# Optimization experiments

Measured on AMD Instinct MI355X. Metric: run time of the kernel, lower is better.

## Reference

```python
import jax, jax.numpy as jnp
import numpy as np

N_NODES = 50000
N_EDGES = 800000
NODE_FEATURES = 128
HIDDEN = 64
N_CLASSES = 6


def gcn_conv(x, src, dst, W, b, n_nodes):
    """PyG GCNConv: out = D^{-1/2}(A+I)D^{-1/2} X W + b (self-loops included)."""
    deg = jax.ops.segment_sum(jnp.ones_like(dst, dtype=x.dtype), dst, num_segments=n_nodes)
    dinv = jnp.where(deg > 0, jax.lax.rsqrt(deg), 0.0)  # [N]
    h = x @ W  # [N, out] - transform before gather (fewer bytes moved)
    norm = dinv[src] * dinv[dst]  # [E+N]
    msg = h[src] * norm[:, None]  # [E+N, out]
    out = jax.ops.segment_sum(msg, dst, num_segments=n_nodes)  # [N, out]
    return out + b


def setup_inputs() -> dict:
    key = jax.random.key(0)
    ks = jax.random.split(key, 8)
    x = jax.random.normal(ks[0], (N_NODES, NODE_FEATURES), dtype=jnp.float32)
    edge_index = jax.random.randint(ks[1], (2, N_EDGES), 0, N_NODES, dtype=jnp.int64)
    W1 = jax.random.normal(ks[2], (NODE_FEATURES, HIDDEN), dtype=jnp.float32) * (1.0 / np.sqrt(NODE_FEATURES))
    b1 = jnp.zeros((HIDDEN,), dtype=jnp.float32)
    W2 = jax.random.normal(ks[3], (HIDDEN, HIDDEN), dtype=jnp.float32) * (1.0 / np.sqrt(HIDDEN))
    b2 = jnp.zeros((HIDDEN,), dtype=jnp.float32)
    Wc = jax.random.normal(ks[4], (HIDDEN * N_NODES, N_CLASSES), dtype=jnp.float32) * (1.0 / np.sqrt(HIDDEN * N_NODES))
    bc = jnp.zeros((N_CLASSES,), dtype=jnp.float32)
    return {"x": x, "edge_index": edge_index, "W1": W1, "b1": b1, "W2": W2, "b2": b2, "Wc": Wc, "bc": bc}


def reference(x, edge_index, W1, b1, W2, b2, Wc, bc):
    n_nodes = x.shape[0]
    loops = jnp.arange(n_nodes, dtype=edge_index.dtype)
    src = jnp.concatenate([edge_index[0], loops])
    dst = jnp.concatenate([edge_index[1], loops])
    h = jax.nn.relu(gcn_conv(x, src, dst, W1, b1, n_nodes))
    h = jax.nn.relu(gcn_conv(h, src, dst, W2, b2, n_nodes))
    logits = h.reshape(1, -1) @ Wc + bc  # [1, n_classes]
    return jax.nn.softmax(logits, axis=1)
```

## Files before the change

kernel.cpp:

```cpp
#include <hip/hip_runtime.h>
#include <math.h>


#define NCH 256
#define RBITS 10
#define NR_MAX 64

__device__ __forceinline__ ushort f32_to_bf16(float f) {
  unsigned u = __float_as_uint(f);
  return (ushort)((u + 0x7fffu + ((u >> 16) & 1u)) >> 16);
}
__device__ __forceinline__ float bf16_to_f32(ushort h) {
  return __uint_as_float(((unsigned)h) << 16);
}


__global__ __launch_bounds__(256) void hist_ranges(
    const int* __restrict__ dst, int* __restrict__ ghist, int NR, int E) {
  __shared__ int h[NR_MAX];
  int tid = threadIdx.x, c = blockIdx.x;
  if (tid < NR) h[tid] = 0;
  __syncthreads();
  int E4 = E >> 2;
  int CH4 = (E4 + NCH - 1) / NCH;
  int i0 = c * CH4, i1 = min(i0 + CH4, E4);
  const int4* d4 = (const int4*)dst;
  for (int i = i0 + tid; i < i1; i += 256) {
    int4 d = d4[i];
    atomicAdd(&h[d.x >> RBITS], 1);
    atomicAdd(&h[d.y >> RBITS], 1);
    atomicAdd(&h[d.z >> RBITS], 1);
    atomicAdd(&h[d.w >> RBITS], 1);
  }
  if (c == NCH - 1) {
    for (int e = (E4 << 2) + tid; e < E; e += 256) atomicAdd(&h[dst[e] >> RBITS], 1);
  }
  __syncthreads();
  if (tid < NR) ghist[tid * NCH + c] = h[tid];
}


__global__ __launch_bounds__(1024) void scan_ghist(int* __restrict__ g, int M) {
  __shared__ int wtot[16];
  int tid = threadIdx.x, lane = tid & 63, wv = tid >> 6;
  int SEG = (M + 1023) >> 10;
  int base = tid * SEG;
  int s = 0;
  for (int k = 0; k < SEG; ++k) { int i = base + k; if (i < M) s += g[i]; }
  int x = s;
#pragma unroll
  for (int d = 1; d < 64; d <<= 1) { int y = __shfl_up(x, d, 64); if (lane >= d) x += y; }
  if (lane == 63) wtot[wv] = x;
  __syncthreads();
  if (wv == 0 && lane < 16) {
    int t = wtot[lane], xx = t;
#pragma unroll
    for (int d = 1; d < 16; d <<= 1) { int y = __shfl_up(xx, d, 64); if (lane >= d) xx += y; }
    wtot[lane] = xx - t;
  }
  __syncthreads();
  int run = x - s + wtot[wv];
  for (int k = 0; k < SEG; ++k) {
    int i = base + k;
    if (i < M) { int tmp = g[i]; g[i] = run; run += tmp; }
  }
}


__global__ __launch_bounds__(256) void scatter_ranges(
    const int* __restrict__ src, const int* __restrict__ dst,
    const int* __restrict__ ghist, int2* __restrict__ ebuf, int NR, int E) {
  __shared__ int cur[NR_MAX];
  int tid = threadIdx.x, c = blockIdx.x;
  if (tid < NR) cur[tid] = ghist[tid * NCH + c];
  __syncthreads();
  int E4 = E >> 2;
  int CH4 = (E4 + NCH - 1) / NCH;
  int i0 = c * CH4, i1 = min(i0 + CH4, E4);
  const int4* d4 = (const int4*)dst;
  const int4* s4 = (const int4*)src;
  for (int i = i0 + tid; i < i1; i += 256) {
    int4 d = d4[i];
    int4 s = s4[i];
    ebuf[atomicAdd(&cur[d.x >> RBITS], 1)] = make_int2(s.x, d.x);
    ebuf[atomicAdd(&cur[d.y >> RBITS], 1)] = make_int2(s.y, d.y);
    ebuf[atomicAdd(&cur[d.z >> RBITS], 1)] = make_int2(s.z, d.z);
    ebuf[atomicAdd(&cur[d.w >> RBITS], 1)] = make_int2(s.w, d.w);
  }
  if (c == NCH - 1) {
    for (int e = (E4 << 2) + tid; e < E; e += 256)
      ebuf[atomicAdd(&cur[dst[e] >> RBITS], 1)] = make_int2(src[e], dst[e]);
  }
}


__global__ __launch_bounds__(1024) void csr_range(
    const int2* __restrict__ ebuf, const int* __restrict__ ghist,
    int* __restrict__ offs, int* __restrict__ srt, float* __restrict__ dinv,
    int N, int E, int NR) {
  __shared__ int hist[1024];
  __shared__ int wtot[16];
  int r = blockIdx.x;
  int lo = r << RBITS;
  int len = min(1024, N - lo);
  int tid = threadIdx.x, lane = tid & 63, wv = tid >> 6;
  int S  = ghist[r * NCH];
  int S1 = (r + 1 < NR) ? ghist[(r + 1) * NCH] : E;
  if (tid < len) hist[tid] = 0;
  __syncthreads();
  for (int i = S + tid; i < S1; i += 1024) atomicAdd(&hist[ebuf[i].y - lo], 1);
  __syncthreads();
  int v = (tid < len) ? hist[tid] : 0;
  if (tid < len) dinv[lo + tid] = rsqrtf((float)(v + 1));
  int x = v;
#pragma unroll
  for (int d = 1; d < 64; d <<= 1) { int y = __shfl_up(x, d, 64); if (lane >= d) x += y; }
  if (lane == 63) wtot[wv] = x;
  __syncthreads();
  if (wv == 0 && lane < 16) {
    int t = wtot[lane], xx = t;
#pragma unroll
    for (int d = 1; d < 16; d <<= 1) { int y = __shfl_up(xx, d, 64); if (lane >= d) xx += y; }
    wtot[lane] = xx - t;
  }
  __syncthreads();
  int excl = x - v + wtot[wv];
  if (tid < len) {
    offs[lo + tid] = S + excl;
    hist[tid] = S + excl;
  }
  if (r == 0 && tid == 0) offs[N] = E;
  __syncthreads();
  for (int i = S + tid; i < S1; i += 1024) {
    int2 e = ebuf[i];
    srt[atomicAdd(&hist[e.y - lo], 1)] = e.x;
  }
}


template <int K, int ROWS>
__global__ __launch_bounds__(256) void gemm_scale(
    const float* __restrict__ X, const float* __restrict__ W,
    const float* __restrict__ dinv, ushort* __restrict__ Gb, int N) {
  __shared__ float smw[K * 64];
  __shared__ float xs[ROWS * K];
  int tid = threadIdx.x, lane = tid & 63, wv = tid >> 6;
  for (int idx = tid; idx < K * 16; idx += 256)
    ((float4*)smw)[idx] = ((const float4*)W)[idx];
  int row0 = blockIdx.x * ROWS;
  int base = row0 * K;
  int cnt4 = (min(ROWS * K, N * K - base)) >> 2;
  const float4* X4 = (const float4*)(X + base);
  for (int idx = tid; idx < cnt4; idx += 256) ((float4*)xs)[idx] = X4[idx];
  __syncthreads();

  constexpr int RW = ROWS / 4;
  float acc[RW];
#pragma unroll
  for (int r = 0; r < RW; ++r) acc[r] = 0.f;
  const float* xr = &xs[(wv * RW) * K];
#pragma unroll 4
  for (int k = 0; k < K; ++k) {
    float wval = smw[k * 64 + lane];
#pragma unroll
    for (int r = 0; r < RW; ++r) acc[r] = fmaf(xr[r * K + k], wval, acc[r]);
  }
#pragma unroll
  for (int r = 0; r < RW; ++r) {
    int row = row0 + wv * RW + r;
    if (row < N) Gb[(size_t)row * 64 + lane] = f32_to_bf16(acc[r] * dinv[row]);
  }
}


__global__ __launch_bounds__(256) void aggregate(
    const ushort* __restrict__ Gb, const int* __restrict__ offs,
    const int* __restrict__ srt, const float* __restrict__ dinv,
    const float* __restrict__ bias, float* __restrict__ H, int N) {
  int lane = threadIdx.x & 63, wv = threadIdx.x >> 6;
  int sub = lane >> 4, fl = lane & 15;
  int node = blockIdx.x * 4 + wv;
  if (node >= N) return;
  const ushort4* G2 = (const ushort4*)Gb;

  int e0 = offs[node], e1 = offs[node + 1];
  int deg = e1 - e0;

  float4 accA = make_float4(0.f, 0.f, 0.f, 0.f);
  float4 accB = make_float4(0.f, 0.f, 0.f, 0.f);
  if (sub == 0) {
    ushort4 q = G2[(size_t)node * 16 + fl];
    accA.x = bf16_to_f32(q.x); accA.y = bf16_to_f32(q.y);
    accA.z = bf16_to_f32(q.z); accA.w = bf16_to_f32(q.w);
  }

  int pre = (deg > 0) ? srt[e0 + min(lane, deg - 1)] : 0;

  int dcap = min(deg, 64);
  int base = 0;
  for (; base + 7 < dcap; base += 8) {
    int sA = __shfl(pre, base + sub, 64);
    int sB = __shfl(pre, base + 4 + sub, 64);
    ushort4 qA = G2[(size_t)sA * 16 + fl];
    ushort4 qB = G2[(size_t)sB * 16 + fl];
    accA.x += bf16_to_f32(qA.x); accA.y += bf16_to_f32(qA.y);
    accA.z += bf16_to_f32(qA.z); accA.w += bf16_to_f32(qA.w);
    accB.x += bf16_to_f32(qB.x); accB.y += bf16_to_f32(qB.y);
    accB.z += bf16_to_f32(qB.z); accB.w += bf16_to_f32(qB.w);
  }
  for (; base + 3 < dcap; base += 4) {
    int s = __shfl(pre, base + sub, 64);
    ushort4 q = G2[(size_t)s * 16 + fl];
    accA.x += bf16_to_f32(q.x); accA.y += bf16_to_f32(q.y);
    accA.z += bf16_to_f32(q.z); accA.w += bf16_to_f32(q.w);
  }
  int e = e0 + base;
  for (; e + 3 < e1; e += 4) {
    int s = srt[e + sub];
    ushort4 q = G2[(size_t)s * 16 + fl];
    accA.x += bf16_to_f32(q.x); accA.y += bf16_to_f32(q.y);
    accA.z += bf16_to_f32(q.z); accA.w += bf16_to_f32(q.w);
  }
  int rem = e1 - e;
  if (sub < rem) {
    int s = srt[e + sub];
    ushort4 q = G2[(size_t)s * 16 + fl];
    accA.x += bf16_to_f32(q.x); accA.y += bf16_to_f32(q.y);
    accA.z += bf16_to_f32(q.z); accA.w += bf16_to_f32(q.w);
  }

  float4 acc;
  acc.x = accA.x + accB.x; acc.y = accA.y + accB.y;
  acc.z = accA.z + accB.z; acc.w = accA.w + accB.w;
#pragma unroll
  for (int m = 16; m < 64; m <<= 1) {
    acc.x += __shfl_xor(acc.x, m, 64);
    acc.y += __shfl_xor(acc.y, m, 64);
    acc.z += __shfl_xor(acc.z, m, 64);
    acc.w += __shfl_xor(acc.w, m, 64);
  }
  if (sub == 0) {
    float dn = dinv[node];
    float4 bb = ((const float4*)bias)[fl];
    float4 r;
    r.x = fmaxf(fmaf(acc.x, dn, bb.x), 0.f);
    r.y = fmaxf(fmaf(acc.y, dn, bb.y), 0.f);
    r.z = fmaxf(fmaf(acc.z, dn, bb.z), 0.f);
    r.w = fmaxf(fmaf(acc.w, dn, bb.w), 0.f);
    ((float4*)H)[(size_t)node * 16 + fl] = r;
  }
}


__global__ __launch_bounds__(256) void classifier(
    const float* __restrict__ H, const float* __restrict__ Wc,
    float* __restrict__ part, int M12) {
  float a[6] = {0.f, 0.f, 0.f, 0.f, 0.f, 0.f};
  int stride = gridDim.x * blockDim.x;
  for (int g = blockIdx.x * blockDim.x + threadIdx.x; g < M12; g += stride) {
    const float4* w4 = (const float4*)Wc + (size_t)g * 3;
    float4 v0 = w4[0];
    float4 v1 = w4[1];
    float4 v2 = w4[2];
    float2 h = ((const float2*)H)[g];
    a[0] = fmaf(h.x, v0.x, a[0]); a[1] = fmaf(h.x, v0.y, a[1]);
    a[2] = fmaf(h.x, v0.z, a[2]); a[3] = fmaf(h.x, v0.w, a[3]);
    a[4] = fmaf(h.x, v1.x, a[4]); a[5] = fmaf(h.x, v1.y, a[5]);
    a[0] = fmaf(h.y, v1.z, a[0]); a[1] = fmaf(h.y, v1.w, a[1]);
    a[2] = fmaf(h.y, v2.x, a[2]); a[3] = fmaf(h.y, v2.y, a[3]);
    a[4] = fmaf(h.y, v2.z, a[4]); a[5] = fmaf(h.y, v2.w, a[5]);
  }
#pragma unroll
  for (int c = 0; c < 6; ++c) {
    for (int d = 32; d > 0; d >>= 1) a[c] += __shfl_down(a[c], d, 64);
  }
  __shared__ float sh[4][6];
  int lane = threadIdx.x & 63, wv = threadIdx.x >> 6;
  if (lane == 0) {
#pragma unroll
    for (int c = 0; c < 6; ++c) sh[wv][c] = a[c];
  }
  __syncthreads();
  if (threadIdx.x == 0) {
#pragma unroll
    for (int c = 0; c < 6; ++c)
      part[(size_t)blockIdx.x * 6 + c] = sh[0][c] + sh[1][c] + sh[2][c] + sh[3][c];
  }
}

__global__ __launch_bounds__(256) void reduce_softmax(
    const float* __restrict__ part, int nb,
    const float* __restrict__ bc, float* __restrict__ out) {
  int tid = threadIdx.x, lane = tid & 63, wv = tid >> 6;
  float a[6] = {0.f, 0.f, 0.f, 0.f, 0.f, 0.f};
  for (int b = tid; b < nb; b += 256) {
    const float* p = part + (size_t)b * 6;
#pragma unroll
    for (int c = 0; c < 6; ++c) a[c] += p[c];
  }
#pragma unroll
  for (int c = 0; c < 6; ++c) {
    for (int d = 32; d > 0; d >>= 1) a[c] += __shfl_down(a[c], d, 64);
  }
  __shared__ float sh[4][6];
  if (lane == 0) {
#pragma unroll
    for (int c = 0; c < 6; ++c) sh[wv][c] = a[c];
  }
  __syncthreads();
  if (tid == 0) {
    float l[6], m = -1e30f;
#pragma unroll
    for (int c = 0; c < 6; ++c) {
      l[c] = sh[0][c] + sh[1][c] + sh[2][c] + sh[3][c] + bc[c];
      m = fmaxf(m, l[c]);
    }
    float s = 0.f;
#pragma unroll
    for (int c = 0; c < 6; ++c) { l[c] = __expf(l[c] - m); s += l[c]; }
    float inv = 1.f / s;
#pragma unroll
    for (int c = 0; c < 6; ++c) out[c] = l[c] * inv;
  }
}


static inline size_t align4up(size_t x) { return (x + 3) & ~(size_t)3; }

extern "C" void kernel_launch(void* const* d_in, const int* in_sizes, int n_in,
                              void* d_out, int out_size, void* d_ws, size_t ws_size,
                              hipStream_t stream) {
  const float* x  = (const float*)d_in[0];
  const int*   ei = (const int*)d_in[1];
  const float* W1 = (const float*)d_in[2];
  const float* b1 = (const float*)d_in[3];
  const float* W2 = (const float*)d_in[4];
  const float* b2 = (const float*)d_in[5];
  const float* Wc = (const float*)d_in[6];
  const float* bc = (const float*)d_in[7];
  float* out = (float*)d_out;

  const int N = in_sizes[0] / 128;
  const int E = in_sizes[1] / 2;
  const int* esrc = ei;
  const int* edst = ei + E;
  const int NR = (N + 1023) >> RBITS;
  const int CGRID = 2048;

  size_t o = 0;
  int* offs   = (int*)d_ws + o;           o = align4up(o + N + 1);
  int* srt    = (int*)d_ws + o;           o = align4up(o + E);
  float* dinv = (float*)d_ws + o;         o = align4up(o + N);
  int* ghist  = (int*)d_ws + o;           o = align4up(o + (size_t)NR * NCH);
  ushort* Gb  = (ushort*)((int*)d_ws + o); o = align4up(o + (size_t)N * 32);
  float* bufB = (float*)d_ws + o;         o = align4up(o + (size_t)N * 64);
  float* part = (float*)d_ws + o;         o = align4up(o + (size_t)CGRID * 6);
  int2* ebuf  = (int2*)bufB;

  hist_ranges<<<NCH, 256, 0, stream>>>(edst, ghist, NR, E);
  scan_ghist<<<1, 1024, 0, stream>>>(ghist, NR * NCH);
  scatter_ranges<<<NCH, 256, 0, stream>>>(esrc, edst, ghist, ebuf, NR, E);
  csr_range<<<NR, 1024, 0, stream>>>(ebuf, ghist, offs, srt, dinv, N, E, NR);

  gemm_scale<128, 32><<<(N + 31) / 32, 256, 0, stream>>>(x, W1, dinv, Gb, N);
  aggregate<<<(N + 3) / 4, 256, 0, stream>>>(Gb, offs, srt, dinv, b1, bufB, N);
  gemm_scale<64, 32><<<(N + 31) / 32, 256, 0, stream>>>(bufB, W2, dinv, Gb, N);
  aggregate<<<(N + 3) / 4, 256, 0, stream>>>(Gb, offs, srt, dinv, b2, bufB, N);

  classifier<<<CGRID, 256, 0, stream>>>(bufB, Wc, part, N * 32);
  reduce_softmax<<<1, 256, 0, stream>>>(part, CGRID, bc, out);
}
```

Before: 165.9 us.

## Split aggregation into two passes by source-node half for cache locality

Each node's CSR neighbor list is partitioned by whether the source index falls in the lower or upper half of nodes, and a split offset is recorded per node. Aggregation then runs as two kernels, the first over low-half sources writing partial fp32 sums and the second over high-half sources accumulating and applying dinv, bias and ReLU. The intent is that each pass gathers from only half of the bf16 feature table (~3.2MB), improving cache hit rates for the random gathers. The cost is extra launches, an fp32 partial-sum write and read per node, and more atomics in CSR construction.

```diff
diff --git a/kernel.cpp b/kernel.cpp
--- a/kernel.cpp
+++ b/kernel.cpp
@@ -96,9 +96,10 @@
 
 __global__ __launch_bounds__(1024) void csr_range(
     const int2* __restrict__ ebuf, const int* __restrict__ ghist,
-    int* __restrict__ offs, int* __restrict__ srt, float* __restrict__ dinv,
-    int N, int E, int NR) {
-  __shared__ int hist[1024];
+    int* __restrict__ offs, int* __restrict__ splits, int* __restrict__ srt,
+    float* __restrict__ dinv, int N, int E, int NR, int NHALF) {
+  __shared__ int hT[1024];
+  __shared__ int hL[1024];
   __shared__ int wtot[16];
   int r = blockIdx.x;
   int lo = r << RBITS;
@@ -106,11 +107,15 @@
   int tid = threadIdx.x, lane = tid & 63, wv = tid >> 6;
   int S  = ghist[r * NCH];
   int S1 = (r + 1 < NR) ? ghist[(r + 1) * NCH] : E;
-  if (tid < len) hist[tid] = 0;
-  __syncthreads();
-  for (int i = S + tid; i < S1; i += 1024) atomicAdd(&hist[ebuf[i].y - lo], 1);
-  __syncthreads();
-  int v = (tid < len) ? hist[tid] : 0;
+  if (tid < len) { hT[tid] = 0; hL[tid] = 0; }
+  __syncthreads();
+  for (int i = S + tid; i < S1; i += 1024) {
+    int2 e = ebuf[i];
+    atomicAdd(&hT[e.y - lo], 1);
+    if (e.x < NHALF) atomicAdd(&hL[e.y - lo], 1);
+  }
+  __syncthreads();
+  int v = (tid < len) ? hT[tid] : 0;
   if (tid < len) dinv[lo + tid] = rsqrtf((float)(v + 1));
   int x = v;
 #pragma unroll
@@ -126,14 +131,20 @@
   __syncthreads();
   int excl = x - v + wtot[wv];
   if (tid < len) {
-    offs[lo + tid] = S + excl;
-    hist[tid] = S + excl;
+    int base = S + excl;
+    int sp = base + hL[tid];
+    offs[lo + tid] = base;
+    splits[lo + tid] = sp;
+    hT[tid] = base;
+    hL[tid] = sp;
   }
   if (r == 0 && tid == 0) offs[N] = E;
   __syncthreads();
   for (int i = S + tid; i < S1; i += 1024) {
     int2 e = ebuf[i];
-    srt[atomicAdd(&hist[e.y - lo], 1)] = e.x;
+    int idx = e.y - lo;
+    int p = (e.x < NHALF) ? atomicAdd(&hT[idx], 1) : atomicAdd(&hL[idx], 1);
+    srt[p] = e.x;
   }
 }
 
@@ -173,25 +184,33 @@
 }
 
 
+template <int PASS>
 __global__ __launch_bounds__(256) void aggregate(
     const ushort* __restrict__ Gb, const int* __restrict__ offs,
-    const int* __restrict__ srt, const float* __restrict__ dinv,
-    const float* __restrict__ bias, float* __restrict__ H, int N) {
+    const int* __restrict__ splits, const int* __restrict__ srt,
+    const float* __restrict__ dinv, const float* __restrict__ bias,
+    float* __restrict__ H, int N) {
   int lane = threadIdx.x & 63, wv = threadIdx.x >> 6;
   int sub = lane >> 4, fl = lane & 15;
   int node = blockIdx.x * 4 + wv;
   if (node >= N) return;
   const ushort4* G2 = (const ushort4*)Gb;
 
-  int e0 = offs[node], e1 = offs[node + 1];
+  int e0, e1;
+  if (PASS == 0) { e0 = offs[node]; e1 = splits[node]; }
+  else           { e0 = splits[node]; e1 = offs[node + 1]; }
   int deg = e1 - e0;
 
   float4 accA = make_float4(0.f, 0.f, 0.f, 0.f);
   float4 accB = make_float4(0.f, 0.f, 0.f, 0.f);
   if (sub == 0) {
-    ushort4 q = G2[(size_t)node * 16 + fl];
-    accA.x = bf16_to_f32(q.x); accA.y = bf16_to_f32(q.y);
-    accA.z = bf16_to_f32(q.z); accA.w = bf16_to_f32(q.w);
+    if (PASS == 0) {
+      ushort4 q = G2[(size_t)node * 16 + fl];
+      accA.x = bf16_to_f32(q.x); accA.y = bf16_to_f32(q.y);
+      accA.z = bf16_to_f32(q.z); accA.w = bf16_to_f32(q.w);
+    } else {
+      accA = ((const float4*)H)[(size_t)node * 16 + fl];
+    }
   }
 
   int pre = (deg > 0) ? srt[e0 + min(lane, deg - 1)] : 0;
@@ -240,14 +259,18 @@
     acc.w += __shfl_xor(acc.w, m, 64);
   }
   if (sub == 0) {
-    float dn = dinv[node];
-    float4 bb = ((const float4*)bias)[fl];
-    float4 r;
-    r.x = fmaxf(fmaf(acc.x, dn, bb.x), 0.f);
-    r.y = fmaxf(fmaf(acc.y, dn, bb.y), 0.f);
-    r.z = fmaxf(fmaf(acc.z, dn, bb.z), 0.f);
-    r.w = fmaxf(fmaf(acc.w, dn, bb.w), 0.f);
-    ((float4*)H)[(size_t)node * 16 + fl] = r;
+    if (PASS == 0) {
+      ((float4*)H)[(size_t)node * 16 + fl] = acc;
+    } else {
+      float dn = dinv[node];
+      float4 bb = ((const float4*)bias)[fl];
+      float4 r;
+      r.x = fmaxf(fmaf(acc.x, dn, bb.x), 0.f);
+      r.y = fmaxf(fmaf(acc.y, dn, bb.y), 0.f);
+      r.z = fmaxf(fmaf(acc.z, dn, bb.z), 0.f);
+      r.w = fmaxf(fmaf(acc.w, dn, bb.w), 0.f);
+      ((float4*)H)[(size_t)node * 16 + fl] = r;
+    }
   }
 }
 
@@ -346,9 +369,11 @@
   const int* edst = ei + E;
   const int NR = (N + 1023) >> RBITS;
   const int CGRID = 2048;
+  const int NHALF = (N / 2 + 3) & ~3;
 
   size_t o = 0;
   int* offs   = (int*)d_ws + o;           o = align4up(o + N + 1);
+  int* splits = (int*)d_ws + o;           o = align4up(o + N);
   int* srt    = (int*)d_ws + o;           o = align4up(o + E);
   float* dinv = (float*)d_ws + o;         o = align4up(o + N);
   int* ghist  = (int*)d_ws + o;           o = align4up(o + (size_t)NR * NCH);
@@ -360,12 +385,15 @@
   hist_ranges<<<NCH, 256, 0, stream>>>(edst, ghist, NR, E);
   scan_ghist<<<1, 1024, 0, stream>>>(ghist, NR * NCH);
   scatter_ranges<<<NCH, 256, 0, stream>>>(esrc, edst, ghist, ebuf, NR, E);
-  csr_range<<<NR, 1024, 0, stream>>>(ebuf, ghist, offs, srt, dinv, N, E, NR);
-
+  csr_range<<<NR, 1024, 0, stream>>>(ebuf, ghist, offs, splits, srt, dinv, N, E, NR, NHALF);
+
+  const int AGRID = (N + 3) / 4;
   gemm_scale<128, 32><<<(N + 31) / 32, 256, 0, stream>>>(x, W1, dinv, Gb, N);
-  aggregate<<<(N + 3) / 4, 256, 0, stream>>>(Gb, offs, srt, dinv, b1, bufB, N);
+  aggregate<0><<<AGRID, 256, 0, stream>>>(Gb, offs, splits, srt, dinv, b1, bufB, N);
+  aggregate<1><<<AGRID, 256, 0, stream>>>(Gb, offs, splits, srt, dinv, b1, bufB, N);
   gemm_scale<64, 32><<<(N + 31) / 32, 256, 0, stream>>>(bufB, W2, dinv, Gb, N);
-  aggregate<<<(N + 3) / 4, 256, 0, stream>>>(Gb, offs, srt, dinv, b2, bufB, N);
+  aggregate<0><<<AGRID, 256, 0, stream>>>(Gb, offs, splits, srt, dinv, b2, bufB, N);
+  aggregate<1><<<AGRID, 256, 0, stream>>>(Gb, offs, splits, srt, dinv, b2, bufB, N);
 
   classifier<<<CGRID, 256, 0, stream>>>(bufB, Wc, part, N * 32);
   reduce_softmax<<<1, 256, 0, stream>>>(part, CGRID, bc, out);
```

Result: slower. 188.7 us (+13.8%).

## Fuse classifier dot product into second aggregation kernel epilogue

Applied to the files above, without the earlier changes.

The second GCN aggregation now applies the bias and ReLU and immediately multiplies each node's 64 features by the matching Wc rows. It reduces the per-block partial logits inside the block and writes them to a partial buffer. This removes the write and re-read of the second-layer hidden matrix and one kernel launch. In exchange the final reduction must sum about 12.5k partials instead of 2048, so it is widened to 1024 threads. Each block also now pays extra shuffle reductions and a __syncthreads.

```diff
diff --git a/kernel.cpp b/kernel.cpp
--- a/kernel.cpp
+++ b/kernel.cpp
@@ -173,22 +173,26 @@
 }
 
 
+template <int CLS>
 __global__ __launch_bounds__(256) void aggregate(
     const ushort* __restrict__ Gb, const int* __restrict__ offs,
     const int* __restrict__ srt, const float* __restrict__ dinv,
-    const float* __restrict__ bias, float* __restrict__ H, int N) {
+    const float* __restrict__ bias, const float* __restrict__ Wc,
+    float* __restrict__ H, float* __restrict__ part, int N) {
   int lane = threadIdx.x & 63, wv = threadIdx.x >> 6;
   int sub = lane >> 4, fl = lane & 15;
   int node = blockIdx.x * 4 + wv;
-  if (node >= N) return;
   const ushort4* G2 = (const ushort4*)Gb;
 
-  int e0 = offs[node], e1 = offs[node + 1];
+  if (CLS == 0 && node >= N) return;
+
+  int e0 = 0, e1 = 0;
+  if (node < N) { e0 = offs[node]; e1 = offs[node + 1]; }
   int deg = e1 - e0;
 
   float4 accA = make_float4(0.f, 0.f, 0.f, 0.f);
   float4 accB = make_float4(0.f, 0.f, 0.f, 0.f);
-  if (sub == 0) {
+  if (sub == 0 && node < N) {
     ushort4 q = G2[(size_t)node * 16 + fl];
     accA.x = bf16_to_f32(q.x); accA.y = bf16_to_f32(q.y);
     accA.z = bf16_to_f32(q.z); accA.w = bf16_to_f32(q.w);
@@ -239,61 +243,61 @@
     acc.z += __shfl_xor(acc.z, m, 64);
     acc.w += __shfl_xor(acc.w, m, 64);
   }
-  if (sub == 0) {
-    float dn = dinv[node];
-    float4 bb = ((const float4*)bias)[fl];
-    float4 r;
-    r.x = fmaxf(fmaf(acc.x, dn, bb.x), 0.f);
-    r.y = fmaxf(fmaf(acc.y, dn, bb.y), 0.f);
-    r.z = fmaxf(fmaf(acc.z, dn, bb.z), 0.f);
-    r.w = fmaxf(fmaf(acc.w, dn, bb.w), 0.f);
-    ((float4*)H)[(size_t)node * 16 + fl] = r;
-  }
-}
-
-
-__global__ __launch_bounds__(256) void classifier(
-    const float* __restrict__ H, const float* __restrict__ Wc,
-    float* __restrict__ part, int M12) {
-  float a[6] = {0.f, 0.f, 0.f, 0.f, 0.f, 0.f};
-  int stride = gridDim.x * blockDim.x;
-  for (int g = blockIdx.x * blockDim.x + threadIdx.x; g < M12; g += stride) {
-    const float4* w4 = (const float4*)Wc + (size_t)g * 3;
-    float4 v0 = w4[0];
-    float4 v1 = w4[1];
-    float4 v2 = w4[2];
-    float2 h = ((const float2*)H)[g];
-    a[0] = fmaf(h.x, v0.x, a[0]); a[1] = fmaf(h.x, v0.y, a[1]);
-    a[2] = fmaf(h.x, v0.z, a[2]); a[3] = fmaf(h.x, v0.w, a[3]);
-    a[4] = fmaf(h.x, v1.x, a[4]); a[5] = fmaf(h.x, v1.y, a[5]);
-    a[0] = fmaf(h.y, v1.z, a[0]); a[1] = fmaf(h.y, v1.w, a[1]);
-    a[2] = fmaf(h.y, v2.x, a[2]); a[3] = fmaf(h.y, v2.y, a[3]);
-    a[4] = fmaf(h.y, v2.z, a[4]); a[5] = fmaf(h.y, v2.w, a[5]);
-  }
-#pragma unroll
-  for (int c = 0; c < 6; ++c) {
-    for (int d = 32; d > 0; d >>= 1) a[c] += __shfl_down(a[c], d, 64);
-  }
-  __shared__ float sh[4][6];
-  int lane = threadIdx.x & 63, wv = threadIdx.x >> 6;
-  if (lane == 0) {
-#pragma unroll
-    for (int c = 0; c < 6; ++c) sh[wv][c] = a[c];
-  }
-  __syncthreads();
-  if (threadIdx.x == 0) {
-#pragma unroll
-    for (int c = 0; c < 6; ++c)
-      part[(size_t)blockIdx.x * 6 + c] = sh[0][c] + sh[1][c] + sh[2][c] + sh[3][c];
-  }
-}
-
-__global__ __launch_bounds__(256) void reduce_softmax(
+
+  if (CLS == 0) {
+    if (sub == 0 && node < N) {
+      float dn = dinv[node];
+      float4 bb = ((const float4*)bias)[fl];
+      float4 r;
+      r.x = fmaxf(fmaf(acc.x, dn, bb.x), 0.f);
+      r.y = fmaxf(fmaf(acc.y, dn, bb.y), 0.f);
+      r.z = fmaxf(fmaf(acc.z, dn, bb.z), 0.f);
+      r.w = fmaxf(fmaf(acc.w, dn, bb.w), 0.f);
+      ((float4*)H)[(size_t)node * 16 + fl] = r;
+    }
+  } else {
+    float a[6] = {0.f, 0.f, 0.f, 0.f, 0.f, 0.f};
+    if (sub == 0 && node < N) {
+      float dn = dinv[node];
+      float4 bb = ((const float4*)bias)[fl];
+      float4 r;
+      r.x = fmaxf(fmaf(acc.x, dn, bb.x), 0.f);
+      r.y = fmaxf(fmaf(acc.y, dn, bb.y), 0.f);
+      r.z = fmaxf(fmaf(acc.z, dn, bb.z), 0.f);
+      r.w = fmaxf(fmaf(acc.w, dn, bb.w), 0.f);
+      const float4* w4 = (const float4*)(Wc + (size_t)node * 384 + fl * 24);
+      float4 w0 = w4[0], w1 = w4[1], w2 = w4[2], w3 = w4[3], w4_ = w4[4], w5 = w4[5];
+      a[0] = fmaf(r.x, w0.x, fmaf(r.y, w1.z, fmaf(r.z, w3.x, r.w * w4_.z)));
+      a[1] = fmaf(r.x, w0.y, fmaf(r.y, w1.w, fmaf(r.z, w3.y, r.w * w4_.w)));
+      a[2] = fmaf(r.x, w0.z, fmaf(r.y, w2.x, fmaf(r.z, w3.z, r.w * w5.x)));
+      a[3] = fmaf(r.x, w0.w, fmaf(r.y, w2.y, fmaf(r.z, w3.w, r.w * w5.y)));
+      a[4] = fmaf(r.x, w1.x, fmaf(r.y, w2.z, fmaf(r.z, w4_.x, r.w * w5.z)));
+      a[5] = fmaf(r.x, w1.y, fmaf(r.y, w2.w, fmaf(r.z, w4_.y, r.w * w5.w)));
+    }
+#pragma unroll
+    for (int c = 0; c < 6; ++c) {
+      for (int d = 32; d > 0; d >>= 1) a[c] += __shfl_down(a[c], d, 64);
+    }
+    __shared__ float sh[4][6];
+    if (lane == 0) {
+#pragma unroll
+      for (int c = 0; c < 6; ++c) sh[wv][c] = a[c];
+    }
+    __syncthreads();
+    if (threadIdx.x == 0) {
+#pragma unroll
+      for (int c = 0; c < 6; ++c)
+        part[(size_t)blockIdx.x * 6 + c] = sh[0][c] + sh[1][c] + sh[2][c] + sh[3][c];
+    }
+  }
+}
+
+__global__ __launch_bounds__(1024) void reduce_softmax(
     const float* __restrict__ part, int nb,
     const float* __restrict__ bc, float* __restrict__ out) {
   int tid = threadIdx.x, lane = tid & 63, wv = tid >> 6;
   float a[6] = {0.f, 0.f, 0.f, 0.f, 0.f, 0.f};
-  for (int b = tid; b < nb; b += 256) {
+  for (int b = tid; b < nb; b += 1024) {
     const float* p = part + (size_t)b * 6;
 #pragma unroll
     for (int c = 0; c < 6; ++c) a[c] += p[c];
@@ -302,7 +306,7 @@
   for (int c = 0; c < 6; ++c) {
     for (int d = 32; d > 0; d >>= 1) a[c] += __shfl_down(a[c], d, 64);
   }
-  __shared__ float sh[4][6];
+  __shared__ float sh[16][6];
   if (lane == 0) {
 #pragma unroll
     for (int c = 0; c < 6; ++c) sh[wv][c] = a[c];
@@ -312,7 +316,9 @@
     float l[6], m = -1e30f;
 #pragma unroll
     for (int c = 0; c < 6; ++c) {
-      l[c] = sh[0][c] + sh[1][c] + sh[2][c] + sh[3][c] + bc[c];
+      float t = 0.f;
+      for (int w = 0; w < 16; ++w) t += sh[w][c];
+      l[c] = t + bc[c];
       m = fmaxf(m, l[c]);
     }
     float s = 0.f;
@@ -345,7 +351,7 @@
   const int* esrc = ei;
   const int* edst = ei + E;
   const int NR = (N + 1023) >> RBITS;
-  const int CGRID = 2048;
+  const int AGRID = (N + 3) / 4;
 
   size_t o = 0;
   int* offs   = (int*)d_ws + o;           o = align4up(o + N + 1);
@@ -354,7 +360,7 @@
   int* ghist  = (int*)d_ws + o;           o = align4up(o + (size_t)NR * NCH);
   ushort* Gb  = (ushort*)((int*)d_ws + o); o = align4up(o + (size_t)N * 32);
   float* bufB = (float*)d_ws + o;         o = align4up(o + (size_t)N * 64);
-  float* part = (float*)d_ws + o;         o = align4up(o + (size_t)CGRID * 6);
+  float* part = (float*)d_ws + o;         o = align4up(o + (size_t)AGRID * 6);
   int2* ebuf  = (int2*)bufB;
 
   hist_ranges<<<NCH, 256, 0, stream>>>(edst, ghist, NR, E);
@@ -363,10 +369,9 @@
   csr_range<<<NR, 1024, 0, stream>>>(ebuf, ghist, offs, srt, dinv, N, E, NR);
 
   gemm_scale<128, 32><<<(N + 31) / 32, 256, 0, stream>>>(x, W1, dinv, Gb, N);
-  aggregate<<<(N + 3) / 4, 256, 0, stream>>>(Gb, offs, srt, dinv, b1, bufB, N);
+  aggregate<0><<<AGRID, 256, 0, stream>>>(Gb, offs, srt, dinv, b1, nullptr, bufB, nullptr, N);
   gemm_scale<64, 32><<<(N + 31) / 32, 256, 0, stream>>>(bufB, W2, dinv, Gb, N);
-  aggregate<<<(N + 3) / 4, 256, 0, stream>>>(Gb, offs, srt, dinv, b2, bufB, N);
-
-  classifier<<<CGRID, 256, 0, stream>>>(bufB, Wc, part, N * 32);
-  reduce_softmax<<<1, 256, 0, stream>>>(part, CGRID, bc, out);
-}
+  aggregate<1><<<AGRID, 256, 0, stream>>>(Gb, offs, srt, dinv, b2, Wc, nullptr, part, N);
+
+  reduce_softmax<<<1, 1024, 0, stream>>>(part, AGRID, bc, out);
+}
```

New measurement: 164.3 us. Within noise of the previous version (-1.0%).
